# Kernel optimization log

Measured on AMD Instinct MI355X. Metric: run time of the kernel, lower is better.

Reference implementation:

```python
import jax, jax.numpy as jnp
import numpy as np

N_NODES = 50000
N_EDGES = 800000
IN_C = 128
HID_C = 128
OUT_C = 128
ATT_H = 64
EPS_COS = 1e-8
EPS_EUD = 1e-6


def _cos_sim(a, b):
    # torch.cosine_similarity(dim=1): dot / max(|a|*|b|, eps)
    num = jnp.sum(a * b, axis=1)
    den = jnp.maximum(jnp.linalg.norm(a, axis=1) * jnp.linalg.norm(b, axis=1), EPS_COS)
    return num / den


def _eud(a, b):
    # nn.PairwiseDistance(p=2): ||a - b + eps||_2
    d = a - b + EPS_EUD
    return jnp.sqrt(jnp.sum(d * d, axis=1))


def _sage(x, row, col, ew, Wl, bl, Wr):
    # SAGEConv with edge weights: mean_j(ew_ij * x_j) @ Wl + bl + x_i @ Wr
    msg = x[col] * ew[:, None]                               # [E, C]
    agg = jax.ops.segment_sum(msg, row, num_segments=N_NODES)  # [N, C]
    deg = jax.ops.segment_sum(jnp.ones_like(ew), row, num_segments=N_NODES)
    agg = agg / jnp.maximum(deg, 1.0)[:, None]
    return agg @ Wl + bl + x @ Wr


def setup_inputs() -> dict:
    key = jax.random.key(0)
    ks = jax.random.split(key, 12)
    s = 0.05
    return {
        "x": jax.random.normal(ks[0], (N_NODES, IN_C), jnp.float32),
        "row": jax.random.randint(ks[1], (N_EDGES,), 0, N_NODES),
        "col": jax.random.randint(ks[2], (N_EDGES,), 0, N_NODES),
        "Wl0": jax.random.normal(ks[3], (IN_C, HID_C), jnp.float32) * s,
        "bl0": jax.random.normal(ks[4], (HID_C,), jnp.float32) * s,
        "Wr0": jax.random.normal(ks[5], (IN_C, HID_C), jnp.float32) * s,
        "Wl1": jax.random.normal(ks[6], (HID_C, OUT_C), jnp.float32) * s,
        "bl1": jax.random.normal(ks[7], (OUT_C,), jnp.float32) * s,
        "Wr1": jax.random.normal(ks[8], (HID_C, OUT_C), jnp.float32) * s,
        "attW1": jax.random.normal(ks[9], (HID_C, ATT_H), jnp.float32) * s,
        "attb1": jax.random.normal(ks[10], (ATT_H,), jnp.float32) * s,
        "attW2": jax.random.normal(ks[11], (ATT_H, 1), jnp.float32) * s,
    }


def reference(x, row, col, Wl0, bl0, Wr0, Wl1, bl1, Wr1, attW1, attb1, attW2):
    xs, xd = x[row], x[col]
    # cosine branch (dropout is a no-op in eval mode)
    e_cos = _cos_sim(xs, xd)
    x3 = jax.nn.relu(_sage(x, row, col, e_cos, Wl0, bl0, Wr0))   # [N, HID]
    e_cos2 = _cos_sim(x3[row], x3[col])
    x1 = _sage(x3, row, col, e_cos2, Wl1, bl1, Wr1)              # [N, OUT]
    # euclidean branch
    e_eud = _eud(xs, xd)
    x4 = jax.nn.relu(_sage(x, row, col, e_eud, Wl0, bl0, Wr0))   # [N, HID]
    e_eud2 = _eud(x4[row], x4[col])
    x2 = _sage(x4, row, col, e_eud2, Wl1, bl1, Wr1)              # [N, OUT]
    # attention pooling over the 4 branch embeddings
    z = jnp.stack([x1, x2, x3, x4], axis=1)                      # [N, 4, C]
    w = jnp.tanh(z @ attW1 + attb1) @ attW2                      # [N, 4, 1]
    beta = jax.nn.softmax(w, axis=1)
    emb = jnp.sum(beta * z, axis=1)                              # [N, C]
    return (emb, x3, x4)
```

## Files before the change

kernel.cpp:

```cpp
#include <hip/hip_runtime.h>

#define NN 50000
#define NE 800000
#define C 128
#define CAP 64
#define CAPSH 6

typedef __attribute__((ext_vector_type(8))) short short8_t;
typedef __attribute__((ext_vector_type(4))) float f32x4;
typedef __attribute__((ext_vector_type(2))) float f32x2;
typedef __attribute__((ext_vector_type(2))) _Float16 half2_t;
typedef __attribute__((ext_vector_type(8))) _Float16 half8_t;

__device__ __forceinline__ unsigned short f2h_u(float f) {
    _Float16 h = (_Float16)f;
    union { _Float16 h; unsigned short u; } v; v.h = h; return v.u;
}

__device__ __forceinline__ float fdot2(half2_t a, half2_t b, float c) {
#if __has_builtin(__builtin_amdgcn_fdot2)
    return __builtin_amdgcn_fdot2(a, b, c, false);
#else
    return c + (float)a.x * (float)b.x + (float)a.y * (float)b.y;
#endif
}

__device__ __forceinline__ float rsq_fast(float x) {
#if __has_builtin(__builtin_amdgcn_rsqf)
    return __builtin_amdgcn_rsqf(x);
#else
    float r; asm volatile("v_rsq_f32 %0, %1" : "=v"(r) : "v"(x)); return r;
#endif
}
__device__ __forceinline__ float sqrt_fast(float x) {
#if __has_builtin(__builtin_amdgcn_sqrtf)
    return __builtin_amdgcn_sqrtf(x);
#else
    float r; asm volatile("v_sqrt_f32 %0, %1" : "=v"(r) : "v"(x)); return r;
#endif
}

template <int CTRL>
__device__ __forceinline__ float dpp_add(float x) {
    int y = __builtin_amdgcn_update_dpp(0, __float_as_int(x), CTRL, 0xF, 0xF, false);
    return x + __int_as_float(y);
}
__device__ __forceinline__ float qred16(float x) {
    x = dpp_add<0xB1>(x);
    x = dpp_add<0x4E>(x);
    x = dpp_add<0x141>(x);
    x = dpp_add<0x140>(x);
    return x;
}

#define BUCK_NB ((NE / 4 + 255) / 256)
#define CAST_NB (NN / 4)
#define PREP_NB ((65536 + 8192) / 256)
__global__ void cast_prep(const float* __restrict__ x, unsigned short* __restrict__ xh,
                          float2* __restrict__ st1,
                          const float* __restrict__ Wl0, const float* __restrict__ Wr0,
                          const float* __restrict__ Wl1, const float* __restrict__ Wr1,
                          const float* __restrict__ aW1,
                          unsigned short* __restrict__ Bt, unsigned short* __restrict__ BtA,
                          const int* __restrict__ row, const int* __restrict__ col,
                          int* __restrict__ cnt, int* __restrict__ colv) {
    if (blockIdx.x < BUCK_NB) {
        int base = (blockIdx.x * 256 + threadIdx.x) * 4;
        if (base < NE) {
            int4 r4 = *(const int4*)(row + base);
            int4 c4 = *(const int4*)(col + base);
            int p0 = atomicAdd(&cnt[r4.x], 1);
            int p1 = atomicAdd(&cnt[r4.y], 1);
            int p2 = atomicAdd(&cnt[r4.z], 1);
            int p3 = atomicAdd(&cnt[r4.w], 1);
            if (p0 < CAP) colv[(r4.x << CAPSH) + p0] = c4.x;
            if (p1 < CAP) colv[(r4.y << CAPSH) + p1] = c4.y;
            if (p2 < CAP) colv[(r4.z << CAPSH) + p2] = c4.z;
            if (p3 < CAP) colv[(r4.w << CAPSH) + p3] = c4.w;
        }
    } else if (blockIdx.x < BUCK_NB + CAST_NB) {
        int node = (blockIdx.x - BUCK_NB) * 4 + (threadIdx.x >> 6);
        int lane = threadIdx.x & 63;
        float2 v = *(const float2*)(x + (size_t)node * C + lane * 2);
        half2_t h; h.x = (_Float16)v.x; h.y = (_Float16)v.y;
        *(half2_t*)(xh + (size_t)node * C + lane * 2) = h;
        float sq = v.x * v.x + v.y * v.y;
        float sm = v.x + v.y;
#pragma unroll
        for (int off = 32; off > 0; off >>= 1) {
            sq += __shfl_xor(sq, off, 64);
            sm += __shfl_xor(sm, off, 64);
        }
        if (lane == 0) st1[node] = make_float2(sq, sm);
    } else {
        int id = (blockIdx.x - BUCK_NB - CAST_NB) * 256 + threadIdx.x;
        if (id < 65536) {
            int layer = id >> 15;
            int c = (id >> 14) & 1;
            int n = (id >> 7) & 127;
            int kk = id & 127;
            const float* W = layer == 0 ? (c == 0 ? Wl0 : Wr0) : (c == 0 ? Wl1 : Wr1);
            Bt[id] = f2h_u(W[kk * 128 + n]);
        } else {
            int a = id - 65536;
            int cl = a >> 7, k = a & 127;
            BtA[a] = f2h_u(aW1[k * 64 + cl]);
        }
    }
}

__global__ __launch_bounds__(256) void fused_l1(
    const unsigned short* __restrict__ xh, const int* __restrict__ colv,
    const int* __restrict__ cnts, const float2* __restrict__ st1,
    unsigned short* __restrict__ aggc, unsigned short* __restrict__ agge) {
    int node = blockIdx.x * 4 + (threadIdx.x >> 6);
    int lane = threadIdx.x & 63;
    int q = lane >> 4, lq = lane & 15;
    int cnt_raw = cnts[node];
    int cnt = cnt_raw < CAP ? cnt_raw : CAP;
    int cv = colv[(node << CAPSH) + lane];
    half8_t xr = *(const half8_t*)(xh + (size_t)node * C + lq * 8);
    float2 sr = st1[node];
    float n2r = sr.x, s1r = sr.y;
    f32x2 ac[4] = {};
    f32x2 ae[4] = {};
    for (int p = 0; p < cnt; p += 4) {
        int ei = p + q;
        bool valid = ei < cnt;
        int src = valid ? ei : (cnt - 1);
        int c0 = __shfl(cv, src, 64);
        half8_t u = *(const half8_t*)(xh + (size_t)c0 * C + lq * 8);
        float2 t0 = st1[c0];
        float d = 0.f;
#pragma unroll
        for (int i = 0; i < 4; ++i) {
            half2_t a; a.x = xr[2 * i]; a.y = xr[2 * i + 1];
            half2_t b; b.x = u[2 * i]; b.y = u[2 * i + 1];
            d = fdot2(a, b, d);
        }
        d = qred16(d);
        float wc0 = d * rsq_fast(fmaxf(n2r * t0.x, 1e-16f));
        float qq = n2r + t0.x - 2.f * d + 2e-6f * (s1r - t0.y) + 1.28e-10f;
        float we0 = sqrt_fast(fmaxf(qq, 0.f));
        if (!valid) { wc0 = 0.f; we0 = 0.f; }
        f32x2 wcv; wcv.x = wc0; wcv.y = wc0;
        f32x2 wev; wev.x = we0; wev.y = we0;
#pragma unroll
        for (int i = 0; i < 4; ++i) {
            f32x2 uf; uf.x = (float)u[2 * i]; uf.y = (float)u[2 * i + 1];
            ac[i] += wcv * uf;
            ae[i] += wev * uf;
        }
    }
#pragma unroll
    for (int i = 0; i < 4; ++i) {
#pragma unroll
        for (int k = 0; k < 2; ++k) {
            float vc = ac[i][k], ve = ae[i][k];
            vc += __shfl_xor(vc, 16, 64);
            vc += __shfl_xor(vc, 32, 64);
            ve += __shfl_xor(ve, 16, 64);
            ve += __shfl_xor(ve, 32, 64);
            ac[i][k] = vc; ae[i][k] = ve;
        }
    }
    if (q == 0) {
        float inv = 1.f / fmaxf((float)cnt_raw, 1.f);
        half8_t hc, he;
#pragma unroll
        for (int i = 0; i < 4; ++i) {
            hc[2 * i]     = (_Float16)(ac[i].x * inv);
            hc[2 * i + 1] = (_Float16)(ac[i].y * inv);
            he[2 * i]     = (_Float16)(ae[i].x * inv);
            he[2 * i + 1] = (_Float16)(ae[i].y * inv);
        }
        *(half8_t*)(aggc + (size_t)node * C + lq * 8) = hc;
        *(half8_t*)(agge + (size_t)node * C + lq * 8) = he;
    }
}

__global__ __launch_bounds__(256) void fused_l2(
    const unsigned short* __restrict__ x34h,
    const int* __restrict__ colv, const int* __restrict__ cnts,
    const float4* __restrict__ st2,
    unsigned short* __restrict__ agg1, unsigned short* __restrict__ agg2) {
    int node = blockIdx.x * 4 + (threadIdx.x >> 6);
    int lane = threadIdx.x & 63;
    int q = lane >> 4, lq = lane & 15;
    int cnt_raw = cnts[node];
    int cnt = cnt_raw < CAP ? cnt_raw : CAP;
    int cv = colv[(node << CAPSH) + lane];
    const unsigned short* nb = x34h + (size_t)node * 256 + lq * 8;
    half8_t x3r = *(const half8_t*)(nb);
    half8_t x4r = *(const half8_t*)(nb + 128);
    float4 sr = st2[node];
    f32x2 a1[4] = {};
    f32x2 a2[4] = {};
    for (int p = 0; p < cnt; p += 4) {
        int ei = p + q;
        bool valid = ei < cnt;
        int src = valid ? ei : (cnt - 1);
        int c0 = __shfl(cv, src, 64);
        const unsigned short* cb = x34h + (size_t)c0 * 256 + lq * 8;
        half8_t u = *(const half8_t*)(cb);
        half8_t v = *(const half8_t*)(cb + 128);
        float4 t0 = st2[c0];
        float d3 = 0.f, d4 = 0.f;
#pragma unroll
        for (int i = 0; i < 4; ++i) {
            half2_t a; a.x = x3r[2 * i]; a.y = x3r[2 * i + 1];
            half2_t b; b.x = u[2 * i]; b.y = u[2 * i + 1];
            d3 = fdot2(a, b, d3);
            half2_t e; e.x = x4r[2 * i]; e.y = x4r[2 * i + 1];
            half2_t f; f.x = v[2 * i]; f.y = v[2 * i + 1];
            d4 = fdot2(e, f, d4);
        }
        d3 = qred16(d3);
        d4 = qred16(d4);
        float wc0 = d3 * rsq_fast(fmaxf(sr.x * t0.x, 1e-16f));
        float qq = sr.y + t0.y - 2.f * d4 + 2e-6f * (sr.z - t0.z) + 1.28e-10f;
        float we0 = sqrt_fast(fmaxf(qq, 0.f));
        if (!valid) { wc0 = 0.f; we0 = 0.f; }
        f32x2 wcv; wcv.x = wc0; wcv.y = wc0;
        f32x2 wev; wev.x = we0; wev.y = we0;
#pragma unroll
        for (int i = 0; i < 4; ++i) {
            f32x2 uf; uf.x = (float)u[2 * i]; uf.y = (float)u[2 * i + 1];
            f32x2 vf; vf.x = (float)v[2 * i]; vf.y = (float)v[2 * i + 1];
            a1[i] += wcv * uf;
            a2[i] += wev * vf;
        }
    }
#pragma unroll
    for (int i = 0; i < 4; ++i) {
#pragma unroll
        for (int k = 0; k < 2; ++k) {
            float v1 = a1[i][k], v2 = a2[i][k];
            v1 += __shfl_xor(v1, 16, 64);
            v1 += __shfl_xor(v1, 32, 64);
            v2 += __shfl_xor(v2, 16, 64);
            v2 += __shfl_xor(v2, 32, 64);
            a1[i][k] = v1; a2[i][k] = v2;
        }
    }
    if (q == 0) {
        float inv = 1.f / fmaxf((float)cnt_raw, 1.f);
        half8_t h1, h2;
#pragma unroll
        for (int i = 0; i < 4; ++i) {
            h1[2 * i]     = (_Float16)(a1[i].x * inv);
            h1[2 * i + 1] = (_Float16)(a1[i].y * inv);
            h2[2 * i]     = (_Float16)(a2[i].x * inv);
            h2[2 * i + 1] = (_Float16)(a2[i].y * inv);
        }
        *(half8_t*)(agg1 + (size_t)node * C + lq * 8) = h1;
        *(half8_t*)(agg2 + (size_t)node * C + lq * 8) = h2;
    }
}

__global__ __launch_bounds__(256) void gemm_dual(
    const unsigned short* __restrict__ A0a, const unsigned short* __restrict__ A0b,
    const unsigned short* __restrict__ A1a, const unsigned short* __restrict__ A1b,
    int a1stride,
    const unsigned short* __restrict__ Bt, const float* __restrict__ bias,
    float* __restrict__ Couta, float* __restrict__ Coutb,
    unsigned short* __restrict__ Chfa, unsigned short* __restrict__ Chfb,
    int chfstride, int relu, float* __restrict__ st2f) {
    __shared__ __align__(16) unsigned short sA[128 * 136];
    __shared__ __align__(16) unsigned short sB[128 * 136];
    const int br = blockIdx.y;
    const unsigned short* A0 = br ? A0b : A0a;
    const unsigned short* A1 = br ? A1b : A1a;
    float* Cout = br ? Coutb : Couta;
    unsigned short* Chf = br ? Chfb : Chfa;
    const int tx = threadIdx.x;
    const int l = tx & 63;
    const int wv = tx >> 6;
    const int wm = wv >> 1, wn = wv & 1;
    const int lr = l & 15;
    const int lq = l >> 4;
    const int n0 = blockIdx.x * 128;

    f32x4 acc[4][4] = {};
    for (int c = 0; c < 2; ++c) {
        const unsigned short* Ac = (c == 0) ? A0 : A1;
        const size_t strideA = (c == 0) ? 128 : a1stride;
#pragma unroll
        for (int it = 0; it < 8; ++it) {
            int idx = it * 256 + tx;
            int r = idx >> 4, s = idx & 15;
            int n = n0 + r; n = n < NN ? n : NN - 1;
            *(short8_t*)(sA + r * 136 + s * 8) = *(const short8_t*)(Ac + (size_t)n * strideA + s * 8);
            *(short8_t*)(sB + r * 136 + s * 8) = *(const short8_t*)(Bt + c * 16384 + idx * 8);
        }
        __syncthreads();
#pragma unroll
        for (int ks = 0; ks < 4; ++ks) {
            half8_t af[4], bfr[4];
#pragma unroll
            for (int t = 0; t < 4; ++t) {
                af[t]  = *(const half8_t*)(sA + (wm * 64 + t * 16 + lr) * 136 + ks * 32 + lq * 8);
                bfr[t] = *(const half8_t*)(sB + (wn * 64 + t * 16 + lr) * 136 + ks * 32 + lq * 8);
            }
#pragma unroll
            for (int mt = 0; mt < 4; ++mt)
#pragma unroll
                for (int nt = 0; nt < 4; ++nt)
                    acc[mt][nt] = __builtin_amdgcn_mfma_f32_16x16x32_f16(af[mt], bfr[nt], acc[mt][nt], 0, 0, 0);
        }
        __syncthreads();
    }
    float* sP2 = (float*)sA;
    float* sP1 = sP2 + 256;
#pragma unroll
    for (int mt = 0; mt < 4; ++mt) {
        int rbase = wm * 64 + mt * 16 + lq * 4;
#pragma unroll
        for (int rg = 0; rg < 4; ++rg) {
            int n = n0 + rbase + rg;
            float s2 = 0.f, s1 = 0.f;
#pragma unroll
            for (int nt = 0; nt < 4; ++nt) {
                int col = wn * 64 + nt * 16 + lr;
                float y = acc[mt][nt][rg] + bias[col];
                if (relu) y = fmaxf(y, 0.f);
                s2 += y * y; s1 += y;
                if (n < NN) {
                    if (Cout) Cout[(size_t)n * 128 + col] = y;
                    Chf[(size_t)n * chfstride + col] = f2h_u(y);
                }
            }
            if (st2f) {
                s2 = qred16(s2);
                s1 = qred16(s1);
                int rloc = rbase + rg;
                if (lr == 0) { sP2[rloc * 2 + wn] = s2; sP1[rloc * 2 + wn] = s1; }
            }
        }
    }
    if (st2f) {
        __syncthreads();
        if (tx < 128) {
            int n = n0 + tx;
            if (n < NN) {
                float q2 = sP2[tx * 2] + sP2[tx * 2 + 1];
                if (br == 0) {
                    st2f[(size_t)n * 4 + 0] = q2;
                } else {
                    st2f[(size_t)n * 4 + 1] = q2;
                    st2f[(size_t)n * 4 + 2] = sP1[tx * 2] + sP1[tx * 2 + 1];
                }
            }
        }
    }
}

__global__ __launch_bounds__(256) void att_fused(
    const unsigned short* __restrict__ x12h, const unsigned short* __restrict__ x34h,
    const unsigned short* __restrict__ BtA, const float* __restrict__ b1,
    const float* __restrict__ W2, float* __restrict__ emb) {
    __shared__ __align__(16) unsigned short sA[128 * 136];
    __shared__ __align__(16) unsigned short sB[64 * 136];
    __shared__ float sW[32][4];
    const int tx = threadIdx.x;
    const int n0 = blockIdx.x * 32;
#pragma unroll
    for (int it = 0; it < 8; ++it) {
        int idx = it * 256 + tx;
        int r = idx >> 4, s = idx & 15;
        int node = n0 + (r >> 2); node = node < NN ? node : NN - 1;
        int b = r & 3;
        const unsigned short* src = (b < 2 ? x12h : x34h) + (size_t)node * 256 + (b & 1) * 128 + s * 8;
        *(short8_t*)(sA + r * 136 + s * 8) = *(const short8_t*)(src);
    }
#pragma unroll
    for (int it = 0; it < 4; ++it) {
        int idx = it * 256 + tx;
        int r = idx >> 4, s = idx & 15;
        *(short8_t*)(sB + r * 136 + s * 8) = *(const short8_t*)(BtA + idx * 8);
    }
    __syncthreads();
    const int w = tx >> 6, lane = tx & 63, lr = lane & 15, lq = lane >> 4;
    f32x4 acc[2][4] = {};
#pragma unroll
    for (int ks = 0; ks < 4; ++ks) {
        half8_t af[2], bfr[4];
#pragma unroll
        for (int mt = 0; mt < 2; ++mt)
            af[mt] = *(const half8_t*)(sA + (w * 32 + mt * 16 + lr) * 136 + ks * 32 + lq * 8);
#pragma unroll
        for (int nt = 0; nt < 4; ++nt)
            bfr[nt] = *(const half8_t*)(sB + (nt * 16 + lr) * 136 + ks * 32 + lq * 8);
#pragma unroll
        for (int mt = 0; mt < 2; ++mt)
#pragma unroll
            for (int nt = 0; nt < 4; ++nt)
                acc[mt][nt] = __builtin_amdgcn_mfma_f32_16x16x32_f16(af[mt], bfr[nt], acc[mt][nt], 0, 0, 0);
    }
#pragma unroll
    for (int mt = 0; mt < 2; ++mt) {
        float part[4] = {0.f, 0.f, 0.f, 0.f};
#pragma unroll
        for (int nt = 0; nt < 4; ++nt) {
            int col = nt * 16 + lr;
            float bb = b1[col], w2 = W2[col];
#pragma unroll
            for (int rg = 0; rg < 4; ++rg) {
                float h = acc[mt][nt][rg] + bb;
                float cl = fminf(fmaxf(h, -15.f), 15.f);
                float e2 = __expf(2.f * cl);
                part[rg] += (e2 - 1.f) / (e2 + 1.f) * w2;
            }
        }
#pragma unroll
        for (int rg = 0; rg < 4; ++rg)
#pragma unroll
            for (int off = 1; off < 16; off <<= 1)
                part[rg] += __shfl_xor(part[rg], off, 64);
        if (lr == 0) {
#pragma unroll
            for (int rg = 0; rg < 4; ++rg) {
                int r = w * 32 + mt * 16 + lq * 4 + rg;
                sW[r >> 2][r & 3] = part[rg];
            }
        }
    }
    __syncthreads();
    int ln = tx >> 3;
    int node = n0 + ln;
    if (node < NN) {
        int ch0 = (tx & 7) * 16;
        float w0 = sW[ln][0], w1 = sW[ln][1], w2 = sW[ln][2], w3 = sW[ln][3];
        float m = fmaxf(fmaxf(w0, w1), fmaxf(w2, w3));
        float e0 = __expf(w0 - m), e1 = __expf(w1 - m), e2 = __expf(w2 - m), e3 = __expf(w3 - m);
        float inv = 1.f / (e0 + e1 + e2 + e3);
        float bt[4] = {e0 * inv, e1 * inv, e2 * inv, e3 * inv};
        float o[16];
#pragma unroll
        for (int i = 0; i < 16; ++i) o[i] = 0.f;
#pragma unroll
        for (int b = 0; b < 4; ++b) {
            int rowoff = (ln * 4 + b) * 136 + ch0;
            half8_t h0 = *(const half8_t*)(sA + rowoff);
            half8_t h1 = *(const half8_t*)(sA + rowoff + 8);
            float bb = bt[b];
#pragma unroll
            for (int i = 0; i < 8; ++i) {
                o[i]     += bb * (float)h0[i];
                o[8 + i] += bb * (float)h1[i];
            }
        }
        float* dst = emb + (size_t)node * 128 + ch0;
#pragma unroll
        for (int i = 0; i < 4; ++i) {
            float4 v4; v4.x = o[4 * i]; v4.y = o[4 * i + 1]; v4.z = o[4 * i + 2]; v4.w = o[4 * i + 3];
            *(float4*)(dst + 4 * i) = v4;
        }
    }
}

extern "C" void kernel_launch(void* const* d_in, const int* in_sizes, int n_in,
                              void* d_out, int out_size, void* d_ws, size_t ws_size,
                              hipStream_t stream) {
    const float* x   = (const float*)d_in[0];
    const int* row   = (const int*)d_in[1];
    const int* col   = (const int*)d_in[2];
    const float* Wl0 = (const float*)d_in[3];
    const float* bl0 = (const float*)d_in[4];
    const float* Wr0 = (const float*)d_in[5];
    const float* Wl1 = (const float*)d_in[6];
    const float* bl1 = (const float*)d_in[7];
    const float* Wr1 = (const float*)d_in[8];
    const float* aW1 = (const float*)d_in[9];
    const float* ab1 = (const float*)d_in[10];
    const float* aW2 = (const float*)d_in[11];

    float* out = (float*)d_out;
    float* emb = out;
    float* x3  = out + (size_t)NN * C;
    float* x4  = out + 2 * (size_t)NN * C;

    char* ws = (char*)d_ws;
    size_t off = 0;
    auto alloc = [&](size_t bytes) -> void* {
        void* p = ws + off;
        off += (bytes + 255) & ~(size_t)255;
        return p;
    };
    int* cnt     = (int*)alloc((size_t)NN * 4);
    int* colv    = (int*)alloc((size_t)NN * CAP * 4);
    float2* st1  = (float2*)alloc((size_t)NN * 8);
    float4* st2  = (float4*)alloc((size_t)NN * 16);
    unsigned short* xh    = (unsigned short*)alloc((size_t)NN * C * 2);
    unsigned short* aggch = (unsigned short*)alloc((size_t)NN * C * 2);
    unsigned short* aggeh = (unsigned short*)alloc((size_t)NN * C * 2);
    unsigned short* x34h  = (unsigned short*)alloc((size_t)NN * 256 * 2);
    unsigned short* x12h  = (unsigned short*)alloc((size_t)NN * 256 * 2);
    unsigned short* Bt    = (unsigned short*)alloc((size_t)65536 * 2);
    unsigned short* BtA   = (unsigned short*)alloc((size_t)8192 * 2);

    hipMemsetAsync(cnt, 0, (size_t)NN * 4, stream);

    cast_prep<<<BUCK_NB + CAST_NB + PREP_NB, 256, 0, stream>>>(
        x, xh, st1, Wl0, Wr0, Wl1, Wr1, aW1, Bt, BtA, row, col, cnt, colv);

    fused_l1<<<NN / 4, 256, 0, stream>>>(xh, colv, cnt, st1, aggch, aggeh);

    const int GB = (NN + 127) / 128;
    gemm_dual<<<dim3(GB, 2), 256, 0, stream>>>(
        aggch, aggeh, xh, xh, 128, Bt, bl0,
        x3, x4, x34h, x34h + 128, 256, 1, (float*)st2);

    fused_l2<<<NN / 4, 256, 0, stream>>>(x34h, colv, cnt, st2, aggch, aggeh);

    gemm_dual<<<dim3(GB, 2), 256, 0, stream>>>(
        aggch, aggeh, x34h, x34h + 128, 256, Bt + 32768, bl1,
        nullptr, nullptr, x12h, x12h + 128, 256, 0, nullptr);

    att_fused<<<(NN + 31) / 32, 256, 0, stream>>>(x12h, x34h, BtA, ab1, aW2, emb);
}
```

Before: 333.7 us.

## Fuse attention scoring into layer GEMMs and drop separate attention kernel

The layer-1 GEMM now also computes the attention scores for x3/x4 from its fp16 output tile held in shared memory. The layer-2 GEMM computes both branches in one block, keeps x1/x2 in LDS, scores them, runs the softmax and writes emb directly. This removes the x12h intermediate, its global round trip and one kernel launch. The cost is fewer blocks for the second GEMM, double the accumulator registers (lower occupancy), and the attention B operand read straight from global memory.

```diff
diff --git a/kernel.cpp b/kernel.cpp
--- a/kernel.cpp
+++ b/kernel.cpp
@@ -258,21 +258,21 @@
     }
 }
 
-__global__ __launch_bounds__(256) void gemm_dual(
+__global__ __launch_bounds__(256) void gemm_l1(
     const unsigned short* __restrict__ A0a, const unsigned short* __restrict__ A0b,
-    const unsigned short* __restrict__ A1a, const unsigned short* __restrict__ A1b,
-    int a1stride,
+    const unsigned short* __restrict__ A1,
     const unsigned short* __restrict__ Bt, const float* __restrict__ bias,
     float* __restrict__ Couta, float* __restrict__ Coutb,
-    unsigned short* __restrict__ Chfa, unsigned short* __restrict__ Chfb,
-    int chfstride, int relu, float* __restrict__ st2f) {
+    unsigned short* __restrict__ x34h,
+    const unsigned short* __restrict__ BtA, const float* __restrict__ ab1,
+    const float* __restrict__ aW2,
+    float* __restrict__ st2f, float* __restrict__ wout) {
     __shared__ __align__(16) unsigned short sA[128 * 136];
     __shared__ __align__(16) unsigned short sB[128 * 136];
     const int br = blockIdx.y;
     const unsigned short* A0 = br ? A0b : A0a;
-    const unsigned short* A1 = br ? A1b : A1a;
     float* Cout = br ? Coutb : Couta;
-    unsigned short* Chf = br ? Chfb : Chfa;
+    unsigned short* Chf = x34h + br * 128;
     const int tx = threadIdx.x;
     const int l = tx & 63;
     const int wv = tx >> 6;
@@ -282,15 +282,15 @@
     const int n0 = blockIdx.x * 128;
 
     f32x4 acc[4][4] = {};
+#pragma unroll
     for (int c = 0; c < 2; ++c) {
         const unsigned short* Ac = (c == 0) ? A0 : A1;
-        const size_t strideA = (c == 0) ? 128 : a1stride;
 #pragma unroll
         for (int it = 0; it < 8; ++it) {
             int idx = it * 256 + tx;
             int r = idx >> 4, s = idx & 15;
             int n = n0 + r; n = n < NN ? n : NN - 1;
-            *(short8_t*)(sA + r * 136 + s * 8) = *(const short8_t*)(Ac + (size_t)n * strideA + s * 8);
+            *(short8_t*)(sA + r * 136 + s * 8) = *(const short8_t*)(Ac + (size_t)n * 128 + s * 8);
             *(short8_t*)(sB + r * 136 + s * 8) = *(const short8_t*)(Bt + c * 16384 + idx * 8);
         }
         __syncthreads();
@@ -317,85 +317,55 @@
         int rbase = wm * 64 + mt * 16 + lq * 4;
 #pragma unroll
         for (int rg = 0; rg < 4; ++rg) {
-            int n = n0 + rbase + rg;
+            int rloc = rbase + rg;
+            int n = n0 + rloc;
             float s2 = 0.f, s1 = 0.f;
 #pragma unroll
             for (int nt = 0; nt < 4; ++nt) {
                 int col = wn * 64 + nt * 16 + lr;
                 float y = acc[mt][nt][rg] + bias[col];
-                if (relu) y = fmaxf(y, 0.f);
+                y = fmaxf(y, 0.f);
                 s2 += y * y; s1 += y;
+                unsigned short hy = f2h_u(y);
+                sB[rloc * 136 + col] = hy;
                 if (n < NN) {
-                    if (Cout) Cout[(size_t)n * 128 + col] = y;
-                    Chf[(size_t)n * chfstride + col] = f2h_u(y);
+                    Cout[(size_t)n * 128 + col] = y;
+                    Chf[(size_t)n * 256 + col] = hy;
                 }
             }
-            if (st2f) {
-                s2 = qred16(s2);
-                s1 = qred16(s1);
-                int rloc = rbase + rg;
-                if (lr == 0) { sP2[rloc * 2 + wn] = s2; sP1[rloc * 2 + wn] = s1; }
-            }
-        }
-    }
-    if (st2f) {
-        __syncthreads();
-        if (tx < 128) {
-            int n = n0 + tx;
-            if (n < NN) {
-                float q2 = sP2[tx * 2] + sP2[tx * 2 + 1];
-                if (br == 0) {
-                    st2f[(size_t)n * 4 + 0] = q2;
-                } else {
-                    st2f[(size_t)n * 4 + 1] = q2;
-                    st2f[(size_t)n * 4 + 2] = sP1[tx * 2] + sP1[tx * 2 + 1];
-                }
-            }
-        }
-    }
-}
-
-__global__ __launch_bounds__(256) void att_fused(
-    const unsigned short* __restrict__ x12h, const unsigned short* __restrict__ x34h,
-    const unsigned short* __restrict__ BtA, const float* __restrict__ b1,
-    const float* __restrict__ W2, float* __restrict__ emb) {
-    __shared__ __align__(16) unsigned short sA[128 * 136];
-    __shared__ __align__(16) unsigned short sB[64 * 136];
-    __shared__ float sW[32][4];
-    const int tx = threadIdx.x;
-    const int n0 = blockIdx.x * 32;
-#pragma unroll
-    for (int it = 0; it < 8; ++it) {
-        int idx = it * 256 + tx;
-        int r = idx >> 4, s = idx & 15;
-        int node = n0 + (r >> 2); node = node < NN ? node : NN - 1;
-        int b = r & 3;
-        const unsigned short* src = (b < 2 ? x12h : x34h) + (size_t)node * 256 + (b & 1) * 128 + s * 8;
-        *(short8_t*)(sA + r * 136 + s * 8) = *(const short8_t*)(src);
-    }
-#pragma unroll
-    for (int it = 0; it < 4; ++it) {
-        int idx = it * 256 + tx;
-        int r = idx >> 4, s = idx & 15;
-        *(short8_t*)(sB + r * 136 + s * 8) = *(const short8_t*)(BtA + idx * 8);
+            s2 = qred16(s2);
+            s1 = qred16(s1);
+            if (lr == 0) { sP2[rloc * 2 + wn] = s2; sP1[rloc * 2 + wn] = s1; }
+        }
     }
     __syncthreads();
-    const int w = tx >> 6, lane = tx & 63, lr = lane & 15, lq = lane >> 4;
-    f32x4 acc[2][4] = {};
+    if (tx < 128) {
+        int n = n0 + tx;
+        if (n < NN) {
+            float q2 = sP2[tx * 2] + sP2[tx * 2 + 1];
+            if (br == 0) {
+                st2f[(size_t)n * 4 + 0] = q2;
+            } else {
+                st2f[(size_t)n * 4 + 1] = q2;
+                st2f[(size_t)n * 4 + 2] = sP1[tx * 2] + sP1[tx * 2 + 1];
+            }
+        }
+    }
+    f32x4 sac[2][4] = {};
 #pragma unroll
     for (int ks = 0; ks < 4; ++ks) {
-        half8_t af[2], bfr[4];
+        half8_t af[2], bf[4];
 #pragma unroll
         for (int mt = 0; mt < 2; ++mt)
-            af[mt] = *(const half8_t*)(sA + (w * 32 + mt * 16 + lr) * 136 + ks * 32 + lq * 8);
+            af[mt] = *(const half8_t*)(sB + (wv * 32 + mt * 16 + lr) * 136 + ks * 32 + lq * 8);
 #pragma unroll
         for (int nt = 0; nt < 4; ++nt)
-            bfr[nt] = *(const half8_t*)(sB + (nt * 16 + lr) * 136 + ks * 32 + lq * 8);
+            bf[nt] = *(const half8_t*)(BtA + (nt * 16 + lr) * 128 + ks * 32 + lq * 8);
 #pragma unroll
         for (int mt = 0; mt < 2; ++mt)
 #pragma unroll
             for (int nt = 0; nt < 4; ++nt)
-                acc[mt][nt] = __builtin_amdgcn_mfma_f32_16x16x32_f16(af[mt], bfr[nt], acc[mt][nt], 0, 0, 0);
+                sac[mt][nt] = __builtin_amdgcn_mfma_f32_16x16x32_f16(af[mt], bf[nt], sac[mt][nt], 0, 0, 0);
     }
 #pragma unroll
     for (int mt = 0; mt < 2; ++mt) {
@@ -403,13 +373,13 @@
 #pragma unroll
         for (int nt = 0; nt < 4; ++nt) {
             int col = nt * 16 + lr;
-            float bb = b1[col], w2 = W2[col];
+            float bb = ab1[col], w2v = aW2[col];
 #pragma unroll
             for (int rg = 0; rg < 4; ++rg) {
-                float h = acc[mt][nt][rg] + bb;
+                float h = sac[mt][nt][rg] + bb;
                 float cl = fminf(fmaxf(h, -15.f), 15.f);
                 float e2 = __expf(2.f * cl);
-                part[rg] += (e2 - 1.f) / (e2 + 1.f) * w2;
+                part[rg] += (e2 - 1.f) / (e2 + 1.f) * w2v;
             }
         }
 #pragma unroll
@@ -420,41 +390,170 @@
         if (lr == 0) {
 #pragma unroll
             for (int rg = 0; rg < 4; ++rg) {
-                int r = w * 32 + mt * 16 + lq * 4 + rg;
-                sW[r >> 2][r & 3] = part[rg];
+                int r = wv * 32 + mt * 16 + lq * 4 + rg;
+                int n = n0 + r;
+                if (n < NN) wout[(size_t)n * 4 + 2 + br] = part[rg];
+            }
+        }
+    }
+}
+
+__global__ __launch_bounds__(256) void gemm2_att(
+    const unsigned short* __restrict__ agg1, const unsigned short* __restrict__ agg2,
+    const unsigned short* __restrict__ x34h,
+    const unsigned short* __restrict__ Bt2, const float* __restrict__ bias,
+    const unsigned short* __restrict__ BtA, const float* __restrict__ ab1,
+    const float* __restrict__ aW2, const float* __restrict__ wout,
+    float* __restrict__ emb) {
+    __shared__ __align__(16) unsigned short sA[128 * 136];
+    __shared__ __align__(16) unsigned short sB[128 * 136];
+    __shared__ float sBeta[128][4];
+    const int tx = threadIdx.x;
+    const int l = tx & 63;
+    const int wv = tx >> 6;
+    const int wm = wv >> 1, wn = wv & 1;
+    const int lr = l & 15;
+    const int lq = l >> 4;
+    const int n0 = blockIdx.x * 128;
+
+    f32x4 acc[2][4][4] = {};
+#pragma unroll
+    for (int br = 0; br < 2; ++br) {
+        const unsigned short* A0 = br ? agg2 : agg1;
+        const unsigned short* A1 = x34h + br * 128;
+#pragma unroll
+        for (int c = 0; c < 2; ++c) {
+            const unsigned short* Ac = (c == 0) ? A0 : A1;
+            const size_t strideA = (c == 0) ? 128 : 256;
+#pragma unroll
+            for (int it = 0; it < 8; ++it) {
+                int idx = it * 256 + tx;
+                int r = idx >> 4, s = idx & 15;
+                int n = n0 + r; n = n < NN ? n : NN - 1;
+                *(short8_t*)(sA + r * 136 + s * 8) = *(const short8_t*)(Ac + (size_t)n * strideA + s * 8);
+                *(short8_t*)(sB + r * 136 + s * 8) = *(const short8_t*)(Bt2 + c * 16384 + idx * 8);
+            }
+            __syncthreads();
+#pragma unroll
+            for (int ks = 0; ks < 4; ++ks) {
+                half8_t af[4], bfr[4];
+#pragma unroll
+                for (int t = 0; t < 4; ++t) {
+                    af[t]  = *(const half8_t*)(sA + (wm * 64 + t * 16 + lr) * 136 + ks * 32 + lq * 8);
+                    bfr[t] = *(const half8_t*)(sB + (wn * 64 + t * 16 + lr) * 136 + ks * 32 + lq * 8);
+                }
+#pragma unroll
+                for (int mt = 0; mt < 4; ++mt)
+#pragma unroll
+                    for (int nt = 0; nt < 4; ++nt)
+                        acc[br][mt][nt] = __builtin_amdgcn_mfma_f32_16x16x32_f16(af[mt], bfr[nt], acc[br][mt][nt], 0, 0, 0);
+            }
+            __syncthreads();
+        }
+    }
+#pragma unroll
+    for (int br = 0; br < 2; ++br) {
+        unsigned short* sY = br ? sB : sA;
+#pragma unroll
+        for (int mt = 0; mt < 4; ++mt) {
+            int rbase = wm * 64 + mt * 16 + lq * 4;
+#pragma unroll
+            for (int nt = 0; nt < 4; ++nt) {
+                int col = wn * 64 + nt * 16 + lr;
+                float bv = bias[col];
+#pragma unroll
+                for (int rg = 0; rg < 4; ++rg)
+                    sY[(rbase + rg) * 136 + col] = f2h_u(acc[br][mt][nt][rg] + bv);
             }
         }
     }
     __syncthreads();
-    int ln = tx >> 3;
-    int node = n0 + ln;
-    if (node < NN) {
-        int ch0 = (tx & 7) * 16;
-        float w0 = sW[ln][0], w1 = sW[ln][1], w2 = sW[ln][2], w3 = sW[ln][3];
-        float m = fmaxf(fmaxf(w0, w1), fmaxf(w2, w3));
-        float e0 = __expf(w0 - m), e1 = __expf(w1 - m), e2 = __expf(w2 - m), e3 = __expf(w3 - m);
-        float inv = 1.f / (e0 + e1 + e2 + e3);
-        float bt[4] = {e0 * inv, e1 * inv, e2 * inv, e3 * inv};
-        float o[16];
-#pragma unroll
-        for (int i = 0; i < 16; ++i) o[i] = 0.f;
-#pragma unroll
-        for (int b = 0; b < 4; ++b) {
-            int rowoff = (ln * 4 + b) * 136 + ch0;
-            half8_t h0 = *(const half8_t*)(sA + rowoff);
-            half8_t h1 = *(const half8_t*)(sA + rowoff + 8);
-            float bb = bt[b];
-#pragma unroll
-            for (int i = 0; i < 8; ++i) {
-                o[i]     += bb * (float)h0[i];
-                o[8 + i] += bb * (float)h1[i];
-            }
-        }
-        float* dst = emb + (size_t)node * 128 + ch0;
-#pragma unroll
-        for (int i = 0; i < 4; ++i) {
-            float4 v4; v4.x = o[4 * i]; v4.y = o[4 * i + 1]; v4.z = o[4 * i + 2]; v4.w = o[4 * i + 3];
-            *(float4*)(dst + 4 * i) = v4;
+    f32x4 sac[2][2][4] = {};
+#pragma unroll
+    for (int ks = 0; ks < 4; ++ks) {
+        half8_t a1f[2], a2f[2], bf[4];
+#pragma unroll
+        for (int mt = 0; mt < 2; ++mt) {
+            a1f[mt] = *(const half8_t*)(sA + (wv * 32 + mt * 16 + lr) * 136 + ks * 32 + lq * 8);
+            a2f[mt] = *(const half8_t*)(sB + (wv * 32 + mt * 16 + lr) * 136 + ks * 32 + lq * 8);
+        }
+#pragma unroll
+        for (int nt = 0; nt < 4; ++nt)
+            bf[nt] = *(const half8_t*)(BtA + (nt * 16 + lr) * 128 + ks * 32 + lq * 8);
+#pragma unroll
+        for (int mt = 0; mt < 2; ++mt)
+#pragma unroll
+            for (int nt = 0; nt < 4; ++nt) {
+                sac[0][mt][nt] = __builtin_amdgcn_mfma_f32_16x16x32_f16(a1f[mt], bf[nt], sac[0][mt][nt], 0, 0, 0);
+                sac[1][mt][nt] = __builtin_amdgcn_mfma_f32_16x16x32_f16(a2f[mt], bf[nt], sac[1][mt][nt], 0, 0, 0);
+            }
+    }
+#pragma unroll
+    for (int b2 = 0; b2 < 2; ++b2) {
+#pragma unroll
+        for (int mt = 0; mt < 2; ++mt) {
+            float part[4] = {0.f, 0.f, 0.f, 0.f};
+#pragma unroll
+            for (int nt = 0; nt < 4; ++nt) {
+                int col = nt * 16 + lr;
+                float bb = ab1[col], w2v = aW2[col];
+#pragma unroll
+                for (int rg = 0; rg < 4; ++rg) {
+                    float h = sac[b2][mt][nt][rg] + bb;
+                    float cl = fminf(fmaxf(h, -15.f), 15.f);
+                    float e2 = __expf(2.f * cl);
+                    part[rg] += (e2 - 1.f) / (e2 + 1.f) * w2v;
+                }
+            }
+#pragma unroll
+            for (int rg = 0; rg < 4; ++rg)
+#pragma unroll
+                for (int off = 1; off < 16; off <<= 1)
+                    part[rg] += __shfl_xor(part[rg], off, 64);
+            if (lr == 0) {
+#pragma unroll
+                for (int rg = 0; rg < 4; ++rg) {
+                    int r = wv * 32 + mt * 16 + lq * 4 + rg;
+                    sBeta[r][b2] = part[rg];
+                }
+            }
+        }
+    }
+    __syncthreads();
+    if (tx < 128) {
+        int n = n0 + tx;
+        float w1 = sBeta[tx][0], w2v = sBeta[tx][1];
+        float w3 = 0.f, w4 = 0.f;
+        if (n < NN) {
+            w3 = wout[(size_t)n * 4 + 2];
+            w4 = wout[(size_t)n * 4 + 3];
+        }
+        float m = fmaxf(fmaxf(w1, w2v), fmaxf(w3, w4));
+        float e1 = __expf(w1 - m), e2 = __expf(w2v - m), e3 = __expf(w3 - m), e4 = __expf(w4 - m);
+        float inv = 1.f / (e1 + e2 + e3 + e4);
+        sBeta[tx][0] = e1 * inv; sBeta[tx][1] = e2 * inv;
+        sBeta[tx][2] = e3 * inv; sBeta[tx][3] = e4 * inv;
+    }
+    __syncthreads();
+#pragma unroll
+    for (int pass = 0; pass < 8; ++pass) {
+        int r = pass * 16 + (tx >> 4);
+        int c0 = (tx & 15) * 8;
+        int n = n0 + r;
+        if (n < NN) {
+            float b1 = sBeta[r][0], b2 = sBeta[r][1], b3 = sBeta[r][2], b4 = sBeta[r][3];
+            half8_t y1 = *(const half8_t*)(sA + r * 136 + c0);
+            half8_t y2 = *(const half8_t*)(sB + r * 136 + c0);
+            half8_t z3 = *(const half8_t*)(x34h + (size_t)n * 256 + c0);
+            half8_t z4 = *(const half8_t*)(x34h + (size_t)n * 256 + 128 + c0);
+            float o[8];
+#pragma unroll
+            for (int i = 0; i < 8; ++i)
+                o[i] = b1 * (float)y1[i] + b2 * (float)y2[i] + b3 * (float)z3[i] + b4 * (float)z4[i];
+            float4 v0; v0.x = o[0]; v0.y = o[1]; v0.z = o[2]; v0.w = o[3];
+            float4 v1; v1.x = o[4]; v1.y = o[5]; v1.z = o[6]; v1.w = o[7];
+            *(float4*)(emb + (size_t)n * 128 + c0) = v0;
+            *(float4*)(emb + (size_t)n * 128 + c0 + 4) = v1;
         }
     }
 }
@@ -495,9 +594,9 @@
     unsigned short* aggch = (unsigned short*)alloc((size_t)NN * C * 2);
     unsigned short* aggeh = (unsigned short*)alloc((size_t)NN * C * 2);
     unsigned short* x34h  = (unsigned short*)alloc((size_t)NN * 256 * 2);
-    unsigned short* x12h  = (unsigned short*)alloc((size_t)NN * 256 * 2);
     unsigned short* Bt    = (unsigned short*)alloc((size_t)65536 * 2);
     unsigned short* BtA   = (unsigned short*)alloc((size_t)8192 * 2);
+    float* wout  = (float*)alloc((size_t)NN * 4 * 4);
 
     hipMemsetAsync(cnt, 0, (size_t)NN * 4, stream);
 
@@ -507,15 +606,13 @@
     fused_l1<<<NN / 4, 256, 0, stream>>>(xh, colv, cnt, st1, aggch, aggeh);
 
     const int GB = (NN + 127) / 128;
-    gemm_dual<<<dim3(GB, 2), 256, 0, stream>>>(
-        aggch, aggeh, xh, xh, 128, Bt, bl0,
-        x3, x4, x34h, x34h + 128, 256, 1, (float*)st2);
+    gemm_l1<<<dim3(GB, 2), 256, 0, stream>>>(
+        aggch, aggeh, xh, Bt, bl0, x3, x4, x34h,
+        BtA, ab1, aW2, (float*)st2, wout);
 
     fused_l2<<<NN / 4, 256, 0, stream>>>(x34h, colv, cnt, st2, aggch, aggeh);
 
-    gemm_dual<<<dim3(GB, 2), 256, 0, stream>>>(
-        aggch, aggeh, x34h, x34h + 128, 256, Bt + 32768, bl1,
-        nullptr, nullptr, x12h, x12h + 128, 256, 0, nullptr);
-
-    att_fused<<<(NN + 31) / 32, 256, 0, stream>>>(x12h, x34h, BtA, ab1, aW2, emb);
-}
+    gemm2_att<<<GB, 256, 0, stream>>>(
+        aggch, aggeh, x34h, Bt + 32768, bl1,
+        BtA, ab1, aW2, wout, emb);
+}
```

Measured after the change: 363.1 us. +8.8%, slower.
